# Performance work log

Measured on AMD Instinct MI355X. Metric: run time of the kernel, lower is better.

The kernel has to match this reference:

```python
import jax, jax.numpy as jnp
import numpy as np

V, D, H, L, FF, B, S = 32000, 1024, 16, 4, 4096, 2, 1024
DK = D // H
STD = 0.02


def setup_inputs() -> dict:
    key = jax.random.key(0)
    ks = jax.random.split(key, 9)
    emb = jax.random.normal(ks[0], (V, D), jnp.float32) * STD
    w_qkv = jax.random.normal(ks[1], (L, D, 3 * D), jnp.float32) * STD
    w_o = jax.random.normal(ks[2], (L, D, D), jnp.float32) * STD
    w_gate = jax.random.normal(ks[3], (L, D, FF), jnp.float32) * STD
    w_up = jax.random.normal(ks[4], (L, D, FF), jnp.float32) * STD
    w_down = jax.random.normal(ks[5], (L, FF, D), jnp.float32) * STD
    norm1_w = jnp.ones((L, D), jnp.float32)
    norm2_w = jnp.ones((L, D), jnp.float32)
    final_norm_w = jnp.ones((D,), jnp.float32)
    input_ids = jax.random.randint(ks[6], (B, S), 0, V, dtype=jnp.int32)
    return dict(input_ids=input_ids, emb=emb, w_qkv=w_qkv, w_o=w_o,
                norm1_w=norm1_w, norm2_w=norm2_w,
                w_gate=w_gate, w_up=w_up, w_down=w_down,
                final_norm_w=final_norm_w)


def _rms(x, w, eps=1e-8):
    return w * x / jnp.sqrt(jnp.mean(x * x, axis=-1, keepdims=True) + eps)


def _rope_factor(seq_len, dk):
    # original: x_rope = x*cos + x*sin with cos/sin of shape [S, dk/2]
    # (duplicated along the feature dim to make the broadcast well-defined)
    pos = jnp.arange(seq_len, dtype=jnp.float32)
    freqs = jnp.exp(jnp.arange(0, dk, 2, dtype=jnp.float32) * (-jnp.log(10000.0) / dk))
    ang = pos[:, None] * freqs[None, :]                     # [S, dk/2]
    c = jnp.cos(ang); s = jnp.sin(ang)
    return jnp.concatenate([c, c], -1) + jnp.concatenate([s, s], -1)  # [S, dk]


def reference(input_ids, emb, w_qkv, w_o, norm1_w, norm2_w, w_gate, w_up, w_down, final_norm_w):
    b, s = input_ids.shape
    d = emb.shape[1]
    x = emb[input_ids] * jnp.sqrt(jnp.float32(d))           # [B,S,D]
    rope = _rope_factor(s, DK)                              # [S,DK]
    causal = jnp.tril(jnp.ones((s, s), bool))
    scale = 1.0 / jnp.sqrt(jnp.float32(DK))

    def block(x, p):
        wqkv, wo, n1, n2, wg, wu, wd = p
        nx = _rms(x, n1)
        qkv = (nx @ wqkv).reshape(b, s, 3, H, DK).transpose(2, 0, 3, 1, 4)  # [3,B,H,S,DK]
        q, k, v = qkv[0], qkv[1], qkv[2]
        q = q * rope
        k = k * rope
        scores = jnp.einsum('bhsd,bhtd->bhst', q, k) * scale
        scores = jnp.where(causal, scores, jnp.float32(-1e9))
        attn = jax.nn.softmax(scores, axis=-1)
        o = jnp.einsum('bhst,bhtd->bhsd', attn, v)
        o = o.transpose(0, 2, 1, 3).reshape(b, s, d)
        x = x + o @ wo
        nx = _rms(x, n2)
        ff = (jax.nn.silu(nx @ wg) * (nx @ wu)) @ wd
        return x + ff, None

    x, _ = jax.lax.scan(block, x, (w_qkv, w_o, norm1_w, norm2_w, w_gate, w_up, w_down))
    x = _rms(x, final_norm_w)
    logits = x @ emb.T                                      # tied lm_head
    return logits
```

## Files before the change

kernel.cpp:

```cpp
#include <hip/hip_runtime.h>
#include <hip/hip_bf16.h>
#include <math.h>

#define B_ 2
#define S_ 1024
#define D_ 1024
#define H_ 16
#define DK_ 64
#define L_ 4
#define FF_ 4096
#define V_ 32000
#define NT (B_*S_)

typedef __attribute__((ext_vector_type(8))) short short8v;
typedef __attribute__((ext_vector_type(4))) float floatx4;
typedef __hip_bfloat16 bf16;

__device__ inline float b2f(unsigned short u) {
  unsigned v = ((unsigned)u) << 16;
  float f; __builtin_memcpy(&f, &v, 4); return f;
}
__device__ inline unsigned short f2bu(float f) {
  bf16 h = __float2bfloat16(f);
  unsigned short u; __builtin_memcpy(&u, &h, 2); return u;
}

__global__ __launch_bounds__(256) void k_embed(const int* __restrict__ ids,
    const float* __restrict__ emb, float* __restrict__ x) {
  int i = blockIdx.x*256 + threadIdx.x;
  if (i >= NT*D_) return;
  int tok = i >> 10;
  int d = i & 1023;
  x[i] = emb[(size_t)ids[tok]*D_ + d] * 32.0f;
}

__global__ __launch_bounds__(256) void k_rms(const float* __restrict__ x,
    const float* __restrict__ w, bf16* __restrict__ o) {
  int row = blockIdx.x;
  const float* xr = x + (size_t)row*D_;
  float s = 0.f;
  for (int d = threadIdx.x; d < D_; d += 256) { float v = xr[d]; s += v*v; }
  for (int off = 32; off; off >>= 1) s += __shfl_down(s, off);
  __shared__ float red[4];
  __shared__ float inv_s;
  int wid = threadIdx.x >> 6;
  if ((threadIdx.x & 63) == 0) red[wid] = s;
  __syncthreads();
  if (threadIdx.x == 0) {
    float t = red[0]+red[1]+red[2]+red[3];
    inv_s = 1.0f / sqrtf(t * (1.0f/D_) + 1e-8f);
  }
  __syncthreads();
  float inv = inv_s;
  bf16* orow = o + (size_t)row*D_;
  for (int d = threadIdx.x; d < D_; d += 256) orow[d] = __float2bfloat16(w[d]*xr[d]*inv);
}

__global__ __launch_bounds__(256) void k_transpose_cast(const float* __restrict__ src0,
    bf16* __restrict__ dst0, int K, int N, size_t src_stride, size_t dst_stride) {
  const float* src = src0 + blockIdx.z * src_stride;
  bf16* dst = dst0 + blockIdx.z * dst_stride;
  __shared__ float t[64][65];
  int k0 = blockIdx.y*64, n0 = blockIdx.x*64;
  int r  = threadIdx.x >> 4;
  int c4 = (threadIdx.x & 15)*4;
  #pragma unroll
  for (int i = 0; i < 4; ++i) {
    float4 v = *(const float4*)(src + (size_t)(k0 + r + i*16)*N + n0 + c4);
    t[r+i*16][c4] = v.x; t[r+i*16][c4+1] = v.y;
    t[r+i*16][c4+2] = v.z; t[r+i*16][c4+3] = v.w;
  }
  __syncthreads();
  int nn = threadIdx.x >> 2;
  int kc = threadIdx.x & 3;
  #pragma unroll
  for (int i = 0; i < 4; ++i) {
    int kk = kc*4 + i*16;
    ushort4 o;
    o.x = f2bu(t[kk][nn]);   o.y = f2bu(t[kk+1][nn]);
    o.z = f2bu(t[kk+2][nn]); o.w = f2bu(t[kk+3][nn]);
    *(ushort4*)(dst + (size_t)(n0+nn)*K + k0 + kk) = o;
  }
}

__global__ __launch_bounds__(256) void k_cast4(const float* __restrict__ s,
    bf16* __restrict__ d, int n4) {
  int i = blockIdx.x*256 + threadIdx.x;
  if (i >= n4) return;
  float4 v = ((const float4*)s)[i];
  ushort4 o;
  o.x = f2bu(v.x); o.y = f2bu(v.y); o.z = f2bu(v.z); o.w = f2bu(v.w);
  ((ushort4*)d)[i] = o;
}

template<int EPI, bool OUTBF>
__global__ __launch_bounds__(256) void k_mfma_gemm_bt(
    const bf16* __restrict__ A, const bf16* __restrict__ Bt,
    const void* __restrict__ aux, void* __restrict__ Cout,
    int M, int N, int K) {
  const int NM = M >> 7, NN = N >> 7;
  const int wg = blockIdx.x;
  const int grp = wg >> 3, xcd = wg & 7;
  const int mi = grp % NM;
  const int ni = xcd + 8*(grp / NM);
  if (ni >= NN) return;
  const int bm = mi * 128;
  const int bn = ni * 128;

  __shared__ bf16 As[128*32];
  __shared__ bf16 Bs[128*32];
  const int tid  = threadIdx.x;
  const int lane = tid & 63;
  const int wave = tid >> 6;
  const int wm = (wave >> 1) * 64;
  const int wn = (wave & 1) * 64;

  floatx4 acc[4][4] = {};

  for (int k0 = 0; k0 < K; k0 += 32) {
    #pragma unroll
    for (int c = 0; c < 2; ++c) {
      int e = (c*256 + tid) * 8;
      int row = e >> 5, col = e & 31;
      const bf16* ga = A  + (size_t)(bm + row)*K + k0 + col;
      const bf16* gb = Bt + (size_t)(bn + row)*K + k0 + col;
      int ldsoff = (c*256 + wave*64) * 8;
      __builtin_amdgcn_global_load_lds(
        (const __attribute__((address_space(1))) void*)ga,
        (__attribute__((address_space(3))) void*)(As + ldsoff), 16, 0, 0);
      __builtin_amdgcn_global_load_lds(
        (const __attribute__((address_space(1))) void*)gb,
        (__attribute__((address_space(3))) void*)(Bs + ldsoff), 16, 0, 0);
    }
    __syncthreads();
    const int r = lane & 15, kc = lane >> 4;
    short8v a[4], b[4];
    #pragma unroll
    for (int i = 0; i < 4; ++i) {
      a[i] = *(const short8v*)(As + (size_t)(wm + i*16 + r)*32 + kc*8);
      b[i] = *(const short8v*)(Bs + (size_t)(wn + i*16 + r)*32 + kc*8);
    }
    #pragma unroll
    for (int i = 0; i < 4; ++i)
      #pragma unroll
      for (int j = 0; j < 4; ++j)
        acc[i][j] = __builtin_amdgcn_mfma_f32_16x16x32_bf16(a[i], b[j], acc[i][j], 0, 0, 0);
    __syncthreads();
  }

  const int cn = lane & 15, rq = lane >> 4;
  #pragma unroll
  for (int i=0;i<4;i++) {
    #pragma unroll
    for (int j=0;j<4;j++) {
      const int gcol = bn + wn + j*16 + cn;
      float freq = 0.f;
      if constexpr (EPI==2) {
        if (gcol < 2048)
          freq = expf((float)(gcol & 31) * -0.28782313662425574f);
      }
      #pragma unroll
      for (int rr=0; rr<4; ++rr) {
        const int grow = bm + wm + i*16 + rq*4 + rr;
        const size_t off = (size_t)grow*N + gcol;
        float v = acc[i][j][rr];
        if constexpr (EPI==1) v += ((const float*)aux)[off];
        if constexpr (EPI==2) {
          if (gcol < 2048) {
            float sn, cs;
            sincosf((float)(grow & 1023) * freq, &sn, &cs);
            v *= (cs + sn);
          }
        }
        if constexpr (OUTBF) ((bf16*)Cout)[off] = __float2bfloat16(v);
        else                 ((float*)Cout)[off] = v;
      }
    }
  }
}

static inline int remap_grid(int M, int N) {
  int NM = M >> 7, NN = N >> 7;
  int NN8 = (NN + 7) & ~7;
  return NM * NN8;
}

__global__ __launch_bounds__(256) void k_gemm_64(
    const bf16* __restrict__ A, const bf16* __restrict__ Bt,
    const float* __restrict__ res, float* __restrict__ C,
    int M, int N, int K, int lda) {
  const int NN = N >> 7;
  const int nwg = gridDim.x;
  const int id = (blockIdx.x & 7)*(nwg >> 3) + (blockIdx.x >> 3);
  const int mi = id / NN, ni = id % NN;
  const int bm = mi << 6, bn = ni << 7;

  __shared__ bf16 As[64*32];
  __shared__ bf16 Bs[128*32];
  const int tid  = threadIdx.x;
  const int lane = tid & 63;
  const int wave = tid >> 6;
  const int wm = (wave >> 1) * 32;
  const int wn = (wave & 1) * 64;

  floatx4 acc[2][4] = {};

  for (int k0 = 0; k0 < K; k0 += 32) {
    {
      int row = tid >> 2, col = (tid & 3)*8;
      const bf16* ga = A + (size_t)(bm + row)*lda + k0 + col;
      __builtin_amdgcn_global_load_lds(
        (const __attribute__((address_space(1))) void*)ga,
        (__attribute__((address_space(3))) void*)(As + wave*512), 16, 0, 0);
    }
    #pragma unroll
    for (int c = 0; c < 2; ++c) {
      int i = c*256 + tid;
      int row = i >> 2, col = (i & 3)*8;
      const bf16* gb = Bt + (size_t)(bn + row)*K + k0 + col;
      __builtin_amdgcn_global_load_lds(
        (const __attribute__((address_space(1))) void*)gb,
        (__attribute__((address_space(3))) void*)(Bs + (c*256 + wave*64)*8), 16, 0, 0);
    }
    __syncthreads();
    const int r = lane & 15, kc = lane >> 4;
    short8v a[2], b[4];
    #pragma unroll
    for (int i = 0; i < 2; ++i)
      a[i] = *(const short8v*)(As + (size_t)(wm + i*16 + r)*32 + kc*8);
    #pragma unroll
    for (int j = 0; j < 4; ++j)
      b[j] = *(const short8v*)(Bs + (size_t)(wn + j*16 + r)*32 + kc*8);
    #pragma unroll
    for (int i = 0; i < 2; ++i)
      #pragma unroll
      for (int j = 0; j < 4; ++j)
        acc[i][j] = __builtin_amdgcn_mfma_f32_16x16x32_bf16(a[i], b[j], acc[i][j], 0, 0, 0);
    __syncthreads();
  }

  const int cn = lane & 15, rq = lane >> 4;
  #pragma unroll
  for (int i = 0; i < 2; ++i) {
    #pragma unroll
    for (int j = 0; j < 4; ++j) {
      #pragma unroll
      for (int rr = 0; rr < 4; ++rr) {
        int grow = bm + wm + i*16 + rq*4 + rr;
        int gcol = bn + wn + j*16 + cn;
        size_t off = (size_t)grow*N + gcol;
        C[off] = acc[i][j][rr] + res[off];
      }
    }
  }
}

template<bool OUTBF>
__global__ __launch_bounds__(512, 2) void k_gemm256(
    const bf16* __restrict__ A, const bf16* __restrict__ Bt,
    void* __restrict__ C, int M, int N, int K) {
  const int NM = M >> 8;
  const int nwg = gridDim.x;
  const int id = (blockIdx.x & 7)*(nwg >> 3) + (blockIdx.x >> 3);
  const int mi = id % NM, ni = id / NM;
  const int bm = mi << 8, bn = ni << 8;

  __shared__ bf16 As3[3][256*32];
  __shared__ bf16 Bs3[3][256*32];

  const int tid  = threadIdx.x;
  const int lane = tid & 63;
  const int wave = tid >> 6;
  const int wr = wave >> 2;
  const int wc = wave & 3;
  const int fr = lane & 15;
  const int kc = lane >> 4;

  floatx4 acc[8][4] = {};
  const int ntk = K >> 5;

  auto stage = [&](int kt, int slot) {
    const bf16* Ab = A  + (size_t)bm*K + kt*32;
    const bf16* Bb = Bt + (size_t)bn*K + kt*32;
    #pragma unroll
    for (int c = 0; c < 2; ++c) {
      int i = c*512 + tid;
      int row = i >> 2, sl = i & 3;
      int gcol = (sl ^ ((row >> 1) & 3)) * 8;
      int ldsoff = (c*512 + wave*64) * 8;
      __builtin_amdgcn_global_load_lds(
        (const __attribute__((address_space(1))) void*)(Ab + (size_t)row*K + gcol),
        (__attribute__((address_space(3))) void*)(&As3[slot][ldsoff]), 16, 0, 0);
      __builtin_amdgcn_global_load_lds(
        (const __attribute__((address_space(1))) void*)(Bb + (size_t)row*K + gcol),
        (__attribute__((address_space(3))) void*)(&Bs3[slot][ldsoff]), 16, 0, 0);
    }
  };

  stage(0, 0);
  if (ntk > 1) stage(1, 1);

  for (int t = 0; t < ntk; ++t) {
    const int cur = t % 3;
    __builtin_amdgcn_sched_barrier(0);
    __builtin_amdgcn_s_barrier();
    __builtin_amdgcn_sched_barrier(0);
    if (t + 2 < ntk) {
      stage(t + 2, (t + 2) % 3);
      __builtin_amdgcn_sched_barrier(0);
      asm volatile("s_waitcnt vmcnt(8)" ::: "memory");
    } else if (t + 1 < ntk) {
      asm volatile("s_waitcnt vmcnt(4)" ::: "memory");
    } else {
      asm volatile("s_waitcnt vmcnt(0)" ::: "memory");
    }
    __builtin_amdgcn_sched_barrier(0);
    __builtin_amdgcn_s_barrier();
    __builtin_amdgcn_sched_barrier(0);

    const bf16* Ab = As3[cur];
    const bf16* Bb = Bs3[cur];
    short8v a[8], b[4];
    #pragma unroll
    for (int f = 0; f < 8; ++f) {
      int r = wr*128 + f*16 + fr;
      int sl = kc ^ ((r >> 1) & 3);
      a[f] = *(const short8v*)(Ab + r*32 + sl*8);
    }
    #pragma unroll
    for (int f = 0; f < 4; ++f) {
      int r = wc*64 + f*16 + fr;
      int sl = kc ^ ((r >> 1) & 3);
      b[f] = *(const short8v*)(Bb + r*32 + sl*8);
    }
    __builtin_amdgcn_s_setprio(1);
    #pragma unroll
    for (int f = 0; f < 8; ++f)
      #pragma unroll
      for (int j = 0; j < 4; ++j)
        acc[f][j] = __builtin_amdgcn_mfma_f32_16x16x32_bf16(a[f], b[j], acc[f][j], 0, 0, 0);
    __builtin_amdgcn_s_setprio(0);
  }

  const int cn = lane & 15, rq = lane >> 4;
  #pragma unroll
  for (int f = 0; f < 8; ++f) {
    #pragma unroll
    for (int j = 0; j < 4; ++j) {
      #pragma unroll
      for (int rr = 0; rr < 4; ++rr) {
        int row = bm + wr*128 + f*16 + rq*4 + rr;
        int col = bn + wc*64 + j*16 + cn;
        size_t off = (size_t)row*N + col;
        if constexpr (OUTBF) ((bf16*)C)[off] = __float2bfloat16(acc[f][j][rr]);
        else                 ((float*)C)[off] = acc[f][j][rr];
      }
    }
  }
}

__global__ __launch_bounds__(256) void k_silumul_gu(bf16* __restrict__ gu) {
  int i = blockIdx.x*256 + threadIdx.x;
  if (i >= NT*512) return;
  int row = i >> 9;
  int c8 = (i & 511)*8;
  unsigned short* p = (unsigned short*)gu + (size_t)row*8192 + c8;
  short8v g = *(const short8v*)p;
  short8v u = *(const short8v*)(p + 4096);
  short8v o;
  #pragma unroll
  for (int j = 0; j < 8; ++j) {
    float gf = b2f((unsigned short)g[j]);
    float uf = b2f((unsigned short)u[j]);
    o[j] = (short)f2bu(gf / (1.0f + expf(-gf)) * uf);
  }
  *(short8v*)p = o;
}

__global__ __launch_bounds__(256) void k_fattn(const bf16* __restrict__ qkvb,
    bf16* __restrict__ outb) {
  const unsigned short* qkv = (const unsigned short*)qkvb;
  const int qt = 15 - blockIdx.x;
  const int h = blockIdx.y, b = blockIdx.z;
  const int tid = threadIdx.x, lane = tid & 63, w = tid >> 6;
  const int g = lane >> 4, qn = lane & 15;

  __shared__ unsigned short Ks[64*64];
  __shared__ unsigned short Vt[64*64];
  __shared__ unsigned short Ps[4*16*64];

  const int q0 = qt * 64;
  const int qw0 = q0 + w*16;

  short8v qf[2];
  {
    const unsigned short* qp = qkv + ((size_t)(b*S_ + qw0 + qn))*3072 + h*DK_ + g*8;
    qf[0] = *(const short8v*)qp;
    qf[1] = *(const short8v*)(qp + 32);
  }

  floatx4 o_acc[4] = {};
  float m_run = -1e30f, l_run = 0.f;

  const int ntile = qt + 1;
  for (int it = 0; it < ntile; ++it) {
    const int t0 = it*64;

    {
      const int trow = w*8 + (lane>>3);
      const int d16 = (lane&7) ^ (trow&7);
      #pragma unroll
      for (int c = 0; c < 2; ++c) {
        const unsigned short* gk = qkv + ((size_t)(b*S_ + t0 + c*32 + trow))*3072
                                   + 1024 + h*DK_ + d16*8;
        __builtin_amdgcn_global_load_lds(
          (const __attribute__((address_space(1))) void*)gk,
          (__attribute__((address_space(3))) void*)(Ks + c*2048 + w*512), 16, 0, 0);
      }
    }
    #pragma unroll
    for (int c = 0; c < 2; ++c) {
      int idx = c*256 + tid;
      int t = idx >> 3;
      int d0 = (idx & 7)*8;
      short8v vv = *(const short8v*)(qkv + ((size_t)(b*S_ + t0 + t))*3072 + 2048 + h*DK_ + d0);
      #pragma unroll
      for (int jj = 0; jj < 8; ++jj) {
        int d = d0 + jj;
        int slot = ((t>>3) ^ (d&7) ^ ((d>>3)&7)) & 7;
        Vt[d*64 + slot*8 + (t&7)] = (unsigned short)vv[jj];
      }
    }
    __syncthreads();

    floatx4 st[4];
    #pragma unroll
    for (int f = 0; f < 4; ++f) {
      st[f] = (floatx4){0.f,0.f,0.f,0.f};
      int t = f*16 + qn;
      #pragma unroll
      for (int ks = 0; ks < 2; ++ks) {
        int slot = ((ks*4 + g) ^ (t&7)) & 7;
        short8v kf = *(const short8v*)(Ks + t*64 + slot*8);
        st[f] = __builtin_amdgcn_mfma_f32_16x16x32_bf16(kf, qf[ks], st[f], 0,0,0);
      }
    }

    const bool diag = (it == qt);
    float sc[4][4];
    #pragma unroll
    for (int f = 0; f < 4; ++f)
      #pragma unroll
      for (int r = 0; r < 4; ++r) {
        float v = st[f][r]*0.125f;
        if (diag) {
          int tl = f*16 + g*4 + r;
          if (tl > w*16 + qn) v = -1e30f;
        }
        sc[f][r] = v;
      }
    float mx = -1e30f;
    #pragma unroll
    for (int f = 0; f < 4; ++f)
      #pragma unroll
      for (int r = 0; r < 4; ++r) mx = fmaxf(mx, sc[f][r]);
    mx = fmaxf(mx, __shfl_xor(mx, 16));
    mx = fmaxf(mx, __shfl_xor(mx, 32));
    float m_new = fmaxf(m_run, mx);
    float corr = __expf(m_run - m_new);
    m_run = m_new;
    float ls = 0.f;
    #pragma unroll
    for (int f = 0; f < 4; ++f)
      #pragma unroll
      for (int r = 0; r < 4; ++r) {
        float p = __expf(sc[f][r] - m_new);
        sc[f][r] = p;
        ls += p;
      }
    ls += __shfl_xor(ls, 16);
    ls += __shfl_xor(ls, 32);
    l_run = l_run*corr + ls;

    unsigned short* Pw = Ps + w*1024;
    #pragma unroll
    for (int f = 0; f < 4; ++f) {
      unsigned int lo = (unsigned int)f2bu(sc[f][0]) | ((unsigned int)f2bu(sc[f][1]) << 16);
      unsigned int hi = (unsigned int)f2bu(sc[f][2]) | ((unsigned int)f2bu(sc[f][3]) << 16);
      int c16 = f*2 + (g>>1);
      int slot = (c16 ^ (qn&7)) & 7;
      *(uint2*)((char*)Pw + qn*128 + slot*16 + (g&1)*8) = make_uint2(lo, hi);
    }

    #pragma unroll
    for (int r = 0; r < 4; ++r) {
      float cr = __shfl(corr, g*4 + r);
      #pragma unroll
      for (int fd = 0; fd < 4; ++fd) o_acc[fd][r] *= cr;
    }

    short8v pf[2];
    #pragma unroll
    for (int ks = 0; ks < 2; ++ks) {
      int slot = ((ks*4 + g) ^ (qn&7)) & 7;
      pf[ks] = *(const short8v*)(Pw + qn*64 + slot*8);
    }
    #pragma unroll
    for (int fd = 0; fd < 4; ++fd) {
      int d = fd*16 + qn;
      #pragma unroll
      for (int ks = 0; ks < 2; ++ks) {
        int slot = ((ks*4 + g) ^ (d&7) ^ ((d>>3)&7)) & 7;
        short8v vf = *(const short8v*)(Vt + d*64 + slot*8);
        o_acc[fd] = __builtin_amdgcn_mfma_f32_16x16x32_bf16(pf[ks], vf, o_acc[fd], 0,0,0);
      }
    }
    __syncthreads();
  }

  float linv = 1.0f / l_run;
  #pragma unroll
  for (int r = 0; r < 4; ++r) {
    float li = __shfl(linv, g*4 + r);
    int row = qw0 + g*4 + r;
    bf16* op = outb + (size_t)(b*S_ + row)*D_ + h*DK_ + qn;
    #pragma unroll
    for (int fd = 0; fd < 4; ++fd)
      op[fd*16] = __float2bfloat16(o_acc[fd][r] * li);
  }
}

extern "C" void kernel_launch(void* const* d_in, const int* in_sizes, int n_in,
                              void* d_out, int out_size, void* d_ws, size_t ws_size,
                              hipStream_t stream) {
  (void)in_sizes; (void)n_in; (void)out_size; (void)ws_size;
  const int*   ids  = (const int*)d_in[0];
  const float* emb  = (const float*)d_in[1];
  const float* wqkv = (const float*)d_in[2];
  const float* wo   = (const float*)d_in[3];
  const float* n1   = (const float*)d_in[4];
  const float* n2   = (const float*)d_in[5];
  const float* wg   = (const float*)d_in[6];
  const float* wu   = (const float*)d_in[7];
  const float* wd   = (const float*)d_in[8];
  const float* fnw  = (const float*)d_in[9];
  float* out = (float*)d_out;

  char* ws = (char*)d_ws;
  float* x      = (float*)ws;                                   ws += (size_t)NT*D_*4;
  bf16*  nx_bf  = (bf16*)ws;                                    ws += (size_t)NT*D_*2;
  bf16*  att_bf = (bf16*)ws;                                    ws += (size_t)NT*D_*2;
  bf16*  shared = (bf16*)ws;                                    ws += (size_t)NT*8192*2;
  bf16*  emb_bf = (bf16*)ws;                                    ws += (size_t)V_*D_*2;
  bf16*  qkv_bf = shared;
  bf16*  gu     = shared;

  bf16* wsc = (bf16*)d_out;
  bf16* wqkv_t = wsc;
  bf16* wo_t   = wqkv_t + (size_t)L_*3*D_*D_;
  bf16* wgu_t  = wo_t   + (size_t)L_*D_*D_;
  bf16* wd_t   = wgu_t  + (size_t)L_*2*D_*FF_;

  dim3 blk(256);

  {
    dim3 gq(3*D_/64, D_/64, L_);
    k_transpose_cast<<<gq, blk, 0, stream>>>(wqkv, wqkv_t, D_, 3*D_,
        (size_t)D_*3*D_, (size_t)3*D_*D_);
    dim3 go(D_/64, D_/64, L_);
    k_transpose_cast<<<go, blk, 0, stream>>>(wo, wo_t, D_, D_,
        (size_t)D_*D_, (size_t)D_*D_);
    dim3 gg(FF_/64, D_/64, L_);
    k_transpose_cast<<<gg, blk, 0, stream>>>(wg, wgu_t, D_, FF_,
        (size_t)D_*FF_, (size_t)2*D_*FF_);
    k_transpose_cast<<<gg, blk, 0, stream>>>(wu, wgu_t + (size_t)FF_*D_, D_, FF_,
        (size_t)D_*FF_, (size_t)2*D_*FF_);
    dim3 gdn(D_/64, FF_/64, L_);
    k_transpose_cast<<<gdn, blk, 0, stream>>>(wd, wd_t, FF_, D_,
        (size_t)FF_*D_, (size_t)D_*FF_);
  }
  k_cast4<<<(V_*D_/4 + 255)/256, blk, 0, stream>>>(emb, emb_bf, V_*D_/4);

  k_embed<<<(NT*D_+255)/256, blk, 0, stream>>>(ids, emb, x);

  for (int l = 0; l < L_; ++l) {
    k_rms<<<NT, blk, 0, stream>>>(x, n1 + (size_t)l*D_, nx_bf);
    k_mfma_gemm_bt<2,true><<<remap_grid(NT,3*D_), blk, 0, stream>>>(
        nx_bf, wqkv_t + (size_t)l*3*D_*D_, nullptr, qkv_bf, NT, 3*D_, D_);
    dim3 gattn(16, H_, B_);
    k_fattn<<<gattn, blk, 0, stream>>>(qkv_bf, att_bf);
    k_gemm_64<<<(NT/64)*(D_/128), blk, 0, stream>>>(
        att_bf, wo_t + (size_t)l*D_*D_, x, x, NT, D_, D_, D_);
    k_rms<<<NT, blk, 0, stream>>>(x, n2 + (size_t)l*D_, nx_bf);
    k_gemm256<true><<<(NT/256)*(2*FF_/256), dim3(512), 0, stream>>>(
        nx_bf, wgu_t + (size_t)l*2*D_*FF_, gu, NT, 2*FF_, D_);
    k_silumul_gu<<<(NT*512 + 255)/256, blk, 0, stream>>>(gu);
    k_gemm_64<<<(NT/64)*(D_/128), blk, 0, stream>>>(
        gu, wd_t + (size_t)l*D_*FF_, x, x, NT, D_, FF_, 2*FF_);
  }
  k_rms<<<NT, blk, 0, stream>>>(x, fnw, nx_bf);
  k_gemm256<false><<<(NT/256)*(V_/256), dim3(512), 0, stream>>>(
      nx_bf, emb_bf, out, NT, V_, D_);
}
```

Before: 1.326 ms.

## Split GEMM k-step into two halves interleaving prefetch chunks with MFMA

The bf16 GEMM main loop now splits each k-step into two phases. Each phase loads half of the A fragments from LDS, issues one chunk of the global-to-LDS prefetch for tile t+2, and runs half of the MFMAs, with a barrier between phases. The wait at loop top changes to vmcnt(4) because one iteration's prefetch is now spread across both phases. The aim is to overlap global loads with compute more evenly and lower register pressure from holding all A fragments at once, at the cost of an extra workgroup barrier per k-step.

```diff
diff --git a/kernel.cpp b/kernel.cpp
--- a/kernel.cpp
+++ b/kernel.cpp
@@ -279,67 +279,79 @@
   floatx4 acc[8][4] = {};
   const int ntk = K >> 5;
 
-  auto stage = [&](int kt, int slot) {
+  auto stage_chunk = [&](int kt, int slot, int c) {
     const bf16* Ab = A  + (size_t)bm*K + kt*32;
     const bf16* Bb = Bt + (size_t)bn*K + kt*32;
-    #pragma unroll
-    for (int c = 0; c < 2; ++c) {
-      int i = c*512 + tid;
-      int row = i >> 2, sl = i & 3;
-      int gcol = (sl ^ ((row >> 1) & 3)) * 8;
-      int ldsoff = (c*512 + wave*64) * 8;
-      __builtin_amdgcn_global_load_lds(
-        (const __attribute__((address_space(1))) void*)(Ab + (size_t)row*K + gcol),
-        (__attribute__((address_space(3))) void*)(&As3[slot][ldsoff]), 16, 0, 0);
-      __builtin_amdgcn_global_load_lds(
-        (const __attribute__((address_space(1))) void*)(Bb + (size_t)row*K + gcol),
-        (__attribute__((address_space(3))) void*)(&Bs3[slot][ldsoff]), 16, 0, 0);
-    }
+    int i = c*512 + tid;
+    int row = i >> 2, sl = i & 3;
+    int gcol = (sl ^ ((row >> 1) & 3)) * 8;
+    int ldsoff = (c*512 + wave*64) * 8;
+    __builtin_amdgcn_global_load_lds(
+      (const __attribute__((address_space(1))) void*)(Ab + (size_t)row*K + gcol),
+      (__attribute__((address_space(3))) void*)(&As3[slot][ldsoff]), 16, 0, 0);
+    __builtin_amdgcn_global_load_lds(
+      (const __attribute__((address_space(1))) void*)(Bb + (size_t)row*K + gcol),
+      (__attribute__((address_space(3))) void*)(&Bs3[slot][ldsoff]), 16, 0, 0);
   };
 
-  stage(0, 0);
-  if (ntk > 1) stage(1, 1);
+  stage_chunk(0, 0, 0); stage_chunk(0, 0, 1);
+  if (ntk > 1) { stage_chunk(1, 1, 0); stage_chunk(1, 1, 1); }
 
   for (int t = 0; t < ntk; ++t) {
     const int cur = t % 3;
-    __builtin_amdgcn_sched_barrier(0);
-    __builtin_amdgcn_s_barrier();
-    __builtin_amdgcn_sched_barrier(0);
-    if (t + 2 < ntk) {
-      stage(t + 2, (t + 2) % 3);
-      __builtin_amdgcn_sched_barrier(0);
-      asm volatile("s_waitcnt vmcnt(8)" ::: "memory");
-    } else if (t + 1 < ntk) {
-      asm volatile("s_waitcnt vmcnt(4)" ::: "memory");
-    } else {
-      asm volatile("s_waitcnt vmcnt(0)" ::: "memory");
-    }
+    if (t + 1 < ntk) asm volatile("s_waitcnt vmcnt(4)" ::: "memory");
+    else             asm volatile("s_waitcnt vmcnt(0)" ::: "memory");
     __builtin_amdgcn_sched_barrier(0);
     __builtin_amdgcn_s_barrier();
     __builtin_amdgcn_sched_barrier(0);
 
     const bf16* Ab = As3[cur];
     const bf16* Bb = Bs3[cur];
-    short8v a[8], b[4];
-    #pragma unroll
-    for (int f = 0; f < 8; ++f) {
+
+    short8v a0[4], b[4];
+    #pragma unroll
+    for (int f = 0; f < 4; ++f) {
       int r = wr*128 + f*16 + fr;
-      int sl = kc ^ ((r >> 1) & 3);
-      a[f] = *(const short8v*)(Ab + r*32 + sl*8);
+      a0[f] = *(const short8v*)(Ab + r*32 + (kc ^ ((r >> 1) & 3))*8);
     }
     #pragma unroll
     for (int f = 0; f < 4; ++f) {
       int r = wc*64 + f*16 + fr;
-      int sl = kc ^ ((r >> 1) & 3);
-      b[f] = *(const short8v*)(Bb + r*32 + sl*8);
-    }
+      b[f] = *(const short8v*)(Bb + r*32 + (kc ^ ((r >> 1) & 3))*8);
+    }
+    if (t + 2 < ntk) stage_chunk(t + 2, (t + 2) % 3, 0);
+    asm volatile("s_waitcnt lgkmcnt(0)" ::: "memory");
+    __builtin_amdgcn_sched_barrier(0);
     __builtin_amdgcn_s_setprio(1);
     #pragma unroll
-    for (int f = 0; f < 8; ++f)
+    for (int f = 0; f < 4; ++f)
       #pragma unroll
       for (int j = 0; j < 4; ++j)
-        acc[f][j] = __builtin_amdgcn_mfma_f32_16x16x32_bf16(a[f], b[j], acc[f][j], 0, 0, 0);
+        acc[f][j] = __builtin_amdgcn_mfma_f32_16x16x32_bf16(a0[f], b[j], acc[f][j], 0, 0, 0);
     __builtin_amdgcn_s_setprio(0);
+    __builtin_amdgcn_sched_barrier(0);
+    __builtin_amdgcn_s_barrier();
+    __builtin_amdgcn_sched_barrier(0);
+
+    short8v a1[4];
+    #pragma unroll
+    for (int f = 0; f < 4; ++f) {
+      int r = wr*128 + (f + 4)*16 + fr;
+      a1[f] = *(const short8v*)(Ab + r*32 + (kc ^ ((r >> 1) & 3))*8);
+    }
+    if (t + 2 < ntk) stage_chunk(t + 2, (t + 2) % 3, 1);
+    asm volatile("s_waitcnt lgkmcnt(0)" ::: "memory");
+    __builtin_amdgcn_sched_barrier(0);
+    __builtin_amdgcn_s_setprio(1);
+    #pragma unroll
+    for (int f = 0; f < 4; ++f)
+      #pragma unroll
+      for (int j = 0; j < 4; ++j)
+        acc[f + 4][j] = __builtin_amdgcn_mfma_f32_16x16x32_bf16(a1[f], b[j], acc[f + 4][j], 0, 0, 0);
+    __builtin_amdgcn_s_setprio(0);
+    __builtin_amdgcn_sched_barrier(0);
+    __builtin_amdgcn_s_barrier();
+    __builtin_amdgcn_sched_barrier(0);
   }
 
   const int cn = lane & 15, rq = lane >> 4;
```

Result: faster. 1.262 ms (-4.8%).
